# Optimization experiments

Measured on AMD Instinct MI355X. Metric: run time of the kernel, lower is better.

## Reference

```python
import jax, jax.numpy as jnp
import numpy as np

NUM_HEADS = 16
EPS = 1e-12  # matches torch F.normalize eps


def _l2_normalize(x):
    n = jnp.sqrt(jnp.sum(x * x, axis=-1, keepdims=True))
    return x / jnp.maximum(n, EPS)


def setup_inputs() -> dict:
    key = jax.random.key(0)
    ks = jax.random.split(key, 9)
    B, L, S, D = 4, 4096, 4096, 1024
    s = 1.0 / np.sqrt(D)
    return {
        "q": jax.random.normal(ks[0], (B, L, D), jnp.float32),
        "k": jax.random.normal(ks[1], (B, S, D), jnp.float32),
        "v": jax.random.normal(ks[2], (B, S, D), jnp.float32),
        "Wq": jax.random.normal(ks[3], (D, D), jnp.float32) * s,
        "bq": jax.random.normal(ks[4], (D,), jnp.float32) * 0.01,
        "Wk": jax.random.normal(ks[5], (D, D), jnp.float32) * s,
        "bk": jax.random.normal(ks[6], (D,), jnp.float32) * 0.01,
        "Wv": jax.random.normal(ks[7], (D, D), jnp.float32) * s,
        "bv": jax.random.normal(ks[8], (D,), jnp.float32) * 0.01,
    }


def reference(q, k, v, Wq, bq, Wk, bk, Wv, bv):
    B = q.shape[0]
    H = NUM_HEADS
    # Linear projections (torch Linear: x @ W^T + b)
    qp = q @ Wq.T + bq  # [B, L, D]
    kp = k @ Wk.T + bk  # [B, S, D]
    vp = v @ Wv.T + bv  # [B, S, D]
    # Split heads: [B, T, H, i] -> [B, H, T, i]
    def split(x):
        Bx, T, D = x.shape
        return x.reshape(Bx, T, H, D // H).transpose(0, 2, 1, 3)
    qh = split(qp)
    kh = _l2_normalize(split(kp))
    vh = _l2_normalize(split(vp))
    # No softmax -> exact reassociation: (q k^T) v == q (k^T v)
    kv = jnp.einsum('bhsi,bhsj->bhij', kh, vh)  # [B, H, i, i]
    xh = jnp.einsum('bhli,bhij->bhlj', qh, kv)  # [B, H, L, i]
    # Merge heads: [B, H, L, i] -> [B, L, H*i]
    Bx, Hh, L, I = xh.shape
    return xh.transpose(0, 2, 1, 3).reshape(Bx, L, Hh * I)
```

## Files before the change

kernel.cpp:

```cpp
#include <hip/hip_runtime.h>
#include <hip/hip_bf16.h>
#include <stdint.h>

typedef __attribute__((ext_vector_type(8))) short bf16x8;
typedef __attribute__((ext_vector_type(4))) float f32x4;
typedef __attribute__((ext_vector_type(8))) unsigned short ushort8;

__device__ __forceinline__ float bf2f(unsigned short u) {
  union { unsigned int i; float f; } x; x.i = ((unsigned int)u) << 16; return x.f;
}
__device__ __forceinline__ unsigned short f2bf(float f) {
  union { __hip_bfloat16 h; unsigned short u; } x; x.h = __float2bfloat16(f); return x.u;
}

__device__ __forceinline__ void gload_lds16(const void* g, void* l) {
  __builtin_amdgcn_global_load_lds((__attribute__((address_space(1))) const void*)g,
                                   (__attribute__((address_space(3))) void*)l, 16, 0, 0);
}

__global__ __launch_bounds__(256) void cvt3_kernel(const float* __restrict__ a,
                                                   const float* __restrict__ b,
                                                   const float* __restrict__ c,
                                                   unsigned short* __restrict__ oa,
                                                   unsigned short* __restrict__ ob,
                                                   unsigned short* __restrict__ oc,
                                                   int n8) {
  const float* in = blockIdx.y == 0 ? a : blockIdx.y == 1 ? b : c;
  unsigned short* out = blockIdx.y == 0 ? oa : blockIdx.y == 1 ? ob : oc;
  int i = blockIdx.x * 256 + threadIdx.x;
  if (i >= n8) return;
  const float4* p = (const float4*)(in + (size_t)i * 8);
  float4 x = p[0], y = p[1];
  ushort8 o;
  o[0] = f2bf(x.x); o[1] = f2bf(x.y); o[2] = f2bf(x.z); o[3] = f2bf(x.w);
  o[4] = f2bf(y.x); o[5] = f2bf(y.y); o[6] = f2bf(y.z); o[7] = f2bf(y.w);
  *(ushort8*)(out + (size_t)i * 8) = o;
}

__device__ __forceinline__ void gemm256_loop(
    const unsigned short* __restrict__ A,
    const unsigned short* __restrict__ B,
    int bm, int bn,
    unsigned short (*As)[256][32], unsigned short (*Bs)[256][32],
    f32x4 (*acc)[4]) {
  const int tid = threadIdx.x;
  const int widx = tid >> 6, lane = tid & 63;
  const int wr = widx >> 2, wc = widx & 3;
  const int fr = lane & 15, fkg = lane >> 4;
  const int pgo = (fkg ^ ((fr >> 1) & 3)) * 8;
  const int srow = lane >> 2;
  const int sg = ((lane & 3) ^ ((lane >> 3) & 3)) * 8;

  const size_t abase = (size_t)(bm * 256) * 1024;
  const size_t bbase = (size_t)(bn * 256) * 1024;

  bf16x8 aF[8], bF[4];

#define STG_A(bufi, kh, kt)                                                                \
  {                                                                                        \
    gload_lds16(A + abase + (size_t)(widx * 16 + srow) * 1024 + (kt) * 64 + (kh) * 32 + sg,\
                &As[(bufi) * 2 + (kh)][widx * 16][0]);                                     \
    gload_lds16(A + abase + (size_t)(128 + widx * 16 + srow) * 1024 + (kt) * 64 + (kh) * 32 + sg, \
                &As[(bufi) * 2 + (kh)][128 + widx * 16][0]);                               \
  }
#define STG_B(bufi, kh, kt)                                                                \
  {                                                                                        \
    gload_lds16(B + bbase + (size_t)(widx * 16 + srow) * 1024 + (kt) * 64 + (kh) * 32 + sg,\
                &Bs[(bufi) * 2 + (kh)][widx * 16][0]);                                     \
    gload_lds16(B + bbase + (size_t)(128 + widx * 16 + srow) * 1024 + (kt) * 64 + (kh) * 32 + sg, \
                &Bs[(bufi) * 2 + (kh)][128 + widx * 16][0]);                               \
  }
#define LDA(bufi, ks)                                                                      \
  _Pragma("unroll") for (int m = 0; m < 8; ++m)                                            \
      aF[m] = *(const bf16x8*)&As[(bufi) * 2 + (ks)][wr * 128 + m * 16 + fr][pgo];
#define LDBALL(bufi, ks)                                                                   \
  _Pragma("unroll") for (int n = 0; n < 4; ++n)                                            \
      bF[n] = *(const bf16x8*)&Bs[(bufi) * 2 + (ks)][wc * 64 + n * 16 + fr][pgo];
#define MMALL()                                                                            \
  {                                                                                        \
    __builtin_amdgcn_s_setprio(1);                                                         \
    _Pragma("unroll") for (int m = 0; m < 8; ++m)                                          \
        _Pragma("unroll") for (int n = 0; n < 4; ++n)                                      \
            acc[m][n] = __builtin_amdgcn_mfma_f32_16x16x32_bf16(aF[m], bF[n], acc[m][n], 0, 0, 0); \
    __builtin_amdgcn_s_setprio(0);                                                         \
  }
#define BARM() asm volatile("s_barrier" ::: "memory")
#define VMW(N) asm volatile("s_waitcnt vmcnt(" #N ")" ::: "memory")

  STG_A(0, 0, 0); STG_B(0, 0, 0);
  STG_A(0, 1, 0); STG_B(0, 1, 0);
  STG_A(1, 0, 1); STG_B(1, 0, 1);
  VMW(4);
  BARM();

  for (int i = 0; i < 8; ++i) {
    const int t1s = 2 * i + 1, u0 = 2 * i + 2, u1 = 2 * i + 3;
    const bool st = (i < 7);
    LDA(0, 0); LDBALL(0, 0); STG_A(1, 1, t1s); STG_B(1, 1, t1s);
    MMALL(); BARM();
    LDA(0, 1); LDBALL(0, 1); if (st) { STG_A(0, 0, u0); STG_B(0, 0, u0); }
    MMALL();
    if (st) { VMW(4); } else { VMW(0); }
    BARM();
    LDA(1, 0); LDBALL(1, 0); if (st) { STG_A(0, 1, u0); STG_B(0, 1, u0); }
    MMALL(); BARM();
    LDA(1, 1); LDBALL(1, 1); if (st) { STG_A(1, 0, u1); STG_B(1, 0, u1); }
    MMALL();
    if (st) { VMW(4); } else { VMW(0); }
    BARM();
  }
#undef STG_A
#undef STG_B
#undef LDA
#undef LDBALL
#undef MMALL
#undef BARM
#undef VMW
}

__global__ __launch_bounds__(512, 1) void proj_norm_kernel(
    const unsigned short* __restrict__ A0, const unsigned short* __restrict__ A1,
    const unsigned short* __restrict__ B0, const unsigned short* __restrict__ B1,
    const float* __restrict__ bias0, const float* __restrict__ bias1,
    unsigned short* __restrict__ C0, unsigned short* __restrict__ C1) {
  __shared__ unsigned short As[4][256][32];
  __shared__ unsigned short Bs[4][256][32];
  const int flat = (blockIdx.z * 64 + blockIdx.y) * 4 + blockIdx.x;
  const int swz = (flat & 7) * 64 + (flat >> 3);
  const int zz = swz >> 8;
  const int rem = swz & 255;
  const int bm = rem >> 2, bn = rem & 3;
  const unsigned short* A = zz ? A1 : A0;
  const unsigned short* B = zz ? B1 : B0;
  const float* bias = zz ? bias1 : bias0;
  unsigned short* C = zz ? C1 : C0;

  f32x4 acc[8][4];
#pragma unroll
  for (int m = 0; m < 8; ++m)
#pragma unroll
    for (int n = 0; n < 4; ++n) acc[m][n] = (f32x4){0.f, 0.f, 0.f, 0.f};

  gemm256_loop(A, B, bm, bn, As, Bs, acc);

  const int tid = threadIdx.x, widx = tid >> 6, lane = tid & 63;
  const int wr = widx >> 2, wc = widx & 3;
  const int fr = lane & 15, g4 = (lane >> 4) * 4;

  float bsv[4];
#pragma unroll
  for (int n = 0; n < 4; ++n) bsv[n] = bias[bn * 256 + wc * 64 + n * 16 + fr];
#pragma unroll
  for (int m = 0; m < 8; ++m) {
    float val[4][4];
    float inv[4];
#pragma unroll
    for (int j = 0; j < 4; ++j) {
      float s = 0.f;
#pragma unroll
      for (int n = 0; n < 4; ++n) {
        val[n][j] = acc[m][n][j] + bsv[n];
        s += val[n][j] * val[n][j];
      }
      s += __shfl_xor(s, 1); s += __shfl_xor(s, 2);
      s += __shfl_xor(s, 4); s += __shfl_xor(s, 8);
      inv[j] = 1.f / fmaxf(sqrtf(s), 1e-12f);
    }
#pragma unroll
    for (int n = 0; n < 4; ++n) {
      const int col = bn * 256 + wc * 64 + n * 16 + fr;
#pragma unroll
      for (int j = 0; j < 4; ++j) {
        const int row = bm * 256 + wr * 128 + m * 16 + g4 + j;
        C[(size_t)row * 1024 + col] = f2bf(val[n][j] * inv[j]);
      }
    }
  }
}

__global__ __launch_bounds__(512, 1) void final_fold_kernel(
    const unsigned short* __restrict__ A,
    const unsigned short* __restrict__ Wqb,
    const float* __restrict__ bq,
    const unsigned short* __restrict__ kvT,
    float* __restrict__ out) {
  __shared__ __align__(16) unsigned char smem[163840];
  unsigned short (*As)[256][32] = (unsigned short (*)[256][32])smem;
  unsigned short (*Bs)[256][32] = (unsigned short (*)[256][32])(smem + 65536);

  const int flat = blockIdx.y * 4 + blockIdx.x;
  const int swz = (flat & 7) * 32 + (flat >> 3);
  const int bm = swz >> 2, bn = swz & 3;
  const int bB = bm >> 4;

  const int tid = threadIdx.x, widx = tid >> 6, lane = tid & 63;
  const int wr = widx >> 2, wc = widx & 3;
  const int fr = lane & 15, fkg = lane >> 4, g4 = fkg * 4;

#pragma unroll
  for (int t = 0; t < 4; ++t) {
    int unit = t * 512 + tid;
    int h = unit >> 9;
    int jr = (unit >> 3) & 63;
    int g = unit & 7;
    ushort8 vvv = *(const ushort8*)(kvT +
        ((size_t)(bB * 16 + bn * 4 + h) * 4096) + jr * 64 + g * 8);
    *(ushort8*)(smem + 131072 + h * 8192 + jr * 128 + ((g ^ (jr & 7)) * 16)) = vvv;
  }
  __syncthreads();

  f32x4 acc[8][4];
#pragma unroll
  for (int m = 0; m < 8; ++m)
#pragma unroll
    for (int n = 0; n < 4; ++n) acc[m][n] = (f32x4){0.f, 0.f, 0.f, 0.f};

  gemm256_loop(A, Wqb, bm, bn, As, Bs, acc);

  {
    float bsv[4];
#pragma unroll
    for (int n = 0; n < 4; ++n) bsv[n] = bq[bn * 256 + wc * 64 + n * 16 + fr];
#pragma unroll
    for (int m = 0; m < 8; ++m)
#pragma unroll
      for (int n = 0; n < 4; ++n)
#pragma unroll
        for (int j = 0; j < 4; ++j) {
          float v = acc[m][n][j] + bsv[n];
          int r = m * 16 + g4 + j;
          int c = n * 16 + fr;
          *(unsigned short*)(smem + widx * 16384 + r * 128 +
                             (((c >> 3) ^ (r & 7)) * 16) + (c & 7) * 2) = f2bf(v);
        }
  }
  __syncthreads();

  f32x4 acc2[8][4];
#pragma unroll
  for (int m = 0; m < 8; ++m)
#pragma unroll
    for (int n = 0; n < 4; ++n) acc2[m][n] = (f32x4){0.f, 0.f, 0.f, 0.f};

#pragma unroll
  for (int ks = 0; ks < 2; ++ks) {
    bf16x8 a2[8], b2[4];
#pragma unroll
    for (int m = 0; m < 8; ++m)
      a2[m] = *(const bf16x8*)(smem + widx * 16384 + (m * 16 + fr) * 128 +
                               (((ks * 4 + fkg) ^ (fr & 7)) * 16));
#pragma unroll
    for (int n = 0; n < 4; ++n)
      b2[n] = *(const bf16x8*)(smem + 131072 + wc * 8192 + (n * 16 + fr) * 128 +
                               (((ks * 4 + fkg) ^ (fr & 7)) * 16));
#pragma unroll
    for (int m = 0; m < 8; ++m)
#pragma unroll
      for (int n = 0; n < 4; ++n)
        acc2[m][n] = __builtin_amdgcn_mfma_f32_16x16x32_bf16(a2[m], b2[n], acc2[m][n], 0, 0, 0);
  }

#pragma unroll
  for (int n = 0; n < 4; ++n) {
    const int col = bn * 256 + wc * 64 + n * 16 + fr;
#pragma unroll
    for (int m = 0; m < 8; ++m)
#pragma unroll
      for (int j = 0; j < 4; ++j) {
        const int row = bm * 256 + wr * 128 + m * 16 + g4 + j;
        out[(size_t)row * 1024 + col] = acc2[m][n][j];
      }
  }
}

__global__ __launch_bounds__(256) void kv_part_kernel(const unsigned short* __restrict__ kh,
                                                      const unsigned short* __restrict__ vh,
                                                      float* __restrict__ kvp) {
  const int chunk = blockIdx.x, h = blockIdx.y, b = blockIdx.z;
  __shared__ unsigned short khT[64][264];
  __shared__ unsigned short vhT[64][264];
  const int tid = threadIdx.x, wid = tid >> 6, lane = tid & 63;
  const int fr = lane & 15, fk = (lane >> 4) * 8, g4 = (lane >> 4) * 4;

  const int jb = tid & 7, sb = tid >> 3;
  const size_t base = ((size_t)b * 4096 + chunk * 256) * 1024 + h * 64;
  {
    ushort8 rk[8], rv[8];
#pragma unroll
    for (int u = 0; u < 8; ++u) {
      rk[u] = *(const ushort8*)(kh + base + (size_t)(sb * 8 + u) * 1024 + jb * 8);
      rv[u] = *(const ushort8*)(vh + base + (size_t)(sb * 8 + u) * 1024 + jb * 8);
    }
#pragma unroll
    for (int jj = 0; jj < 8; ++jj) {
      ushort8 ck, cv;
#pragma unroll
      for (int u = 0; u < 8; ++u) { ck[u] = rk[u][jj]; cv[u] = rv[u][jj]; }
      *(ushort8*)&khT[jb * 8 + jj][sb * 8] = ck;
      *(ushort8*)&vhT[jb * 8 + jj][sb * 8] = cv;
    }
  }
  __syncthreads();

  f32x4 acc2[4];
#pragma unroll
  for (int n = 0; n < 4; ++n) acc2[n] = (f32x4){0.f, 0.f, 0.f, 0.f};
#pragma unroll
  for (int ks = 0; ks < 8; ++ks) {
    bf16x8 a2 = *(const bf16x8*)&khT[wid * 16 + fr][ks * 32 + fk];
    bf16x8 b2[4];
#pragma unroll
    for (int jt = 0; jt < 4; ++jt) b2[jt] = *(const bf16x8*)&vhT[jt * 16 + fr][ks * 32 + fk];
#pragma unroll
    for (int jt = 0; jt < 4; ++jt)
      acc2[jt] = __builtin_amdgcn_mfma_f32_16x16x32_bf16(a2, b2[jt], acc2[jt], 0, 0, 0);
  }
  float* dst = kvp + ((size_t)chunk * 64 + b * 16 + h) * 4096;
#pragma unroll
  for (int jt = 0; jt < 4; ++jt)
#pragma unroll
    for (int jj = 0; jj < 4; ++jj)
      dst[(wid * 16 + g4 + jj) * 64 + jt * 16 + fr] = acc2[jt][jj];
}

__global__ __launch_bounds__(256) void kvt_reduce_kernel(const float* __restrict__ kvp,
                                                         unsigned short* __restrict__ kvT) {
  const int bh = blockIdx.x;
  for (int e = threadIdx.x; e < 4096; e += 256) {
    float s = 0.f;
#pragma unroll
    for (int c = 0; c < 16; ++c) s += kvp[((size_t)c * 64 + bh) * 4096 + e];
    int i = e >> 6, j = e & 63;
    kvT[(size_t)bh * 4096 + j * 64 + i] = f2bf(s);
  }
}

extern "C" void kernel_launch(void* const* d_in, const int* in_sizes, int n_in,
                              void* d_out, int out_size, void* d_ws, size_t ws_size,
                              hipStream_t stream) {
  const float* q = (const float*)d_in[0];
  const float* k = (const float*)d_in[1];
  const float* v = (const float*)d_in[2];
  const float* Wq = (const float*)d_in[3];
  const float* bq = (const float*)d_in[4];
  const float* Wk = (const float*)d_in[5];
  const float* bk = (const float*)d_in[6];
  const float* Wv = (const float*)d_in[7];
  const float* bv = (const float*)d_in[8];
  float* out = (float*)d_out;

  const size_t NE = (size_t)16384 * 1024;
  const size_t MB = 1048576;

  char* ws = (char*)d_ws;
  unsigned short* kbf = (unsigned short*)(ws + 0 * MB);
  unsigned short* qbf = (unsigned short*)(ws + 32 * MB);
  unsigned short* kh = (unsigned short*)(ws + 64 * MB);
  unsigned short* vh = (unsigned short*)(ws + 96 * MB);
  unsigned short* vbf = (unsigned short*)(ws + 64 * MB);
  unsigned short* Wqb = (unsigned short*)(ws + 128 * MB);
  unsigned short* Wkb = (unsigned short*)(ws + 130 * MB);
  unsigned short* Wvb = (unsigned short*)(ws + 132 * MB);
  unsigned short* kvT = (unsigned short*)(ws + 134 * MB);
  float* kvp = (float*)kbf;

  (void)vbf;

  unsigned short* kbf_ = (unsigned short*)(ws + 0 * MB);
  unsigned short* vbf_ = (unsigned short*)(ws + 32 * MB);
  unsigned short* qbf_ = vbf_;

  cvt3_kernel<<<dim3(8192, 2), 256, 0, stream>>>(k, v, v, kbf_, vbf_, vbf_, (int)(NE / 8));
  cvt3_kernel<<<dim3(512, 3), 256, 0, stream>>>(Wq, Wk, Wv, Wqb, Wkb, Wvb, 131072);

  proj_norm_kernel<<<dim3(4, 64, 2), 512, 0, stream>>>(kbf_, vbf_, Wkb, Wvb, bk, bv, kh, vh);

  cvt3_kernel<<<dim3(8192, 1), 256, 0, stream>>>(q, q, q, qbf_, qbf_, qbf_, (int)(NE / 8));

  kv_part_kernel<<<dim3(16, 16, 4), 256, 0, stream>>>(kh, vh, kvp);

  kvt_reduce_kernel<<<64, 256, 0, stream>>>(kvp, kvT);

  final_fold_kernel<<<dim3(4, 64), 512, 0, stream>>>(qbf_, Wqb, bq, kvT, out);
}
```

Baseline: 212.0 us.

## Rewrite projection+norm GEMM with simple double-buffered LDS loop

Replaces the shared 4-stage hand-scheduled gemm256_loop in proj_norm_kernel with a standalone 2-buffer loop. Each iteration issues the next tile's direct global-to-LDS loads, then does fragment reads and MFMAs under raised priority, with one barrier per k-step. LDS use drops from 4 stages to 2. The new loads also drop the XOR swizzle, so fragment reads may hit LDS bank conflicts. The launch bound asks for 4 blocks per CU, which will not fit given the large accumulator register use. Host code is only tidied, with pointer aliases renamed.

```diff
diff --git a/kernel.cpp b/kernel.cpp
--- a/kernel.cpp
+++ b/kernel.cpp
@@ -37,6 +37,103 @@
   *(ushort8*)(out + (size_t)i * 8) = o;
 }
 
+__global__ __launch_bounds__(512, 4) void proj_norm_kernel(
+    const unsigned short* __restrict__ A0, const unsigned short* __restrict__ A1,
+    const unsigned short* __restrict__ B0, const unsigned short* __restrict__ B1,
+    const float* __restrict__ bias0, const float* __restrict__ bias1,
+    unsigned short* __restrict__ C0, unsigned short* __restrict__ C1) {
+  __shared__ unsigned short As[2][256][32];
+  __shared__ unsigned short Bs[2][256][32];
+
+  const int flat = (blockIdx.z * 64 + blockIdx.y) * 4 + blockIdx.x;
+  const int swz = (flat & 7) * 64 + (flat >> 3);
+  const int zz = swz >> 8;
+  const int rem = swz & 255;
+  const int bm = rem >> 2, bn = rem & 3;
+  const unsigned short* A = zz ? A1 : A0;
+  const unsigned short* B = zz ? B1 : B0;
+  const float* bias = zz ? bias1 : bias0;
+  unsigned short* C = zz ? C1 : C0;
+
+  const int tid = threadIdx.x, widx = tid >> 6, lane = tid & 63;
+  const int wr = widx >> 2, wc = widx & 3;
+  const int fr = lane & 15, fkg = lane >> 4, g4 = fkg * 4;
+  const int srow = lane >> 2;
+  const int sgr = (lane & 3) * 8;
+
+  const size_t abase = (size_t)(bm * 256) * 1024;
+  const size_t bbase = (size_t)(bn * 256) * 1024;
+
+  f32x4 acc[8][4];
+#pragma unroll
+  for (int m = 0; m < 8; ++m)
+#pragma unroll
+    for (int n = 0; n < 4; ++n) acc[m][n] = (f32x4){0.f, 0.f, 0.f, 0.f};
+
+#define STG(buf, kt)                                                                       \
+  _Pragma("unroll") for (int cc = 0; cc < 2; ++cc) {                                       \
+    const int r0 = cc * 128 + widx * 16;                                                   \
+    gload_lds16(A + abase + (size_t)(r0 + srow) * 1024 + (kt) * 32 + sgr,                  \
+                &As[buf][r0][0]);                                                          \
+    gload_lds16(B + bbase + (size_t)(r0 + srow) * 1024 + (kt) * 32 + sgr,                  \
+                &Bs[buf][r0][0]);                                                          \
+  }
+
+  STG(0, 0);
+  __syncthreads();
+
+  for (int t = 0; t < 32; ++t) {
+    const int cur = t & 1;
+    if (t < 31) { STG(cur ^ 1, t + 1); }
+    bf16x8 aF[8], bF[4];
+#pragma unroll
+    for (int m = 0; m < 8; ++m)
+      aF[m] = *(const bf16x8*)&As[cur][wr * 128 + m * 16 + fr][fkg * 8];
+#pragma unroll
+    for (int n = 0; n < 4; ++n)
+      bF[n] = *(const bf16x8*)&Bs[cur][wc * 64 + n * 16 + fr][fkg * 8];
+    __builtin_amdgcn_s_setprio(1);
+#pragma unroll
+    for (int m = 0; m < 8; ++m)
+#pragma unroll
+      for (int n = 0; n < 4; ++n)
+        acc[m][n] = __builtin_amdgcn_mfma_f32_16x16x32_bf16(aF[m], bF[n], acc[m][n], 0, 0, 0);
+    __builtin_amdgcn_s_setprio(0);
+    __syncthreads();
+  }
+#undef STG
+
+  float bsv[4];
+#pragma unroll
+  for (int n = 0; n < 4; ++n) bsv[n] = bias[bn * 256 + wc * 64 + n * 16 + fr];
+#pragma unroll
+  for (int m = 0; m < 8; ++m) {
+    float val[4][4];
+    float inv[4];
+#pragma unroll
+    for (int j = 0; j < 4; ++j) {
+      float s = 0.f;
+#pragma unroll
+      for (int n = 0; n < 4; ++n) {
+        val[n][j] = acc[m][n][j] + bsv[n];
+        s += val[n][j] * val[n][j];
+      }
+      s += __shfl_xor(s, 1); s += __shfl_xor(s, 2);
+      s += __shfl_xor(s, 4); s += __shfl_xor(s, 8);
+      inv[j] = 1.f / fmaxf(sqrtf(s), 1e-12f);
+    }
+#pragma unroll
+    for (int n = 0; n < 4; ++n) {
+      const int col = bn * 256 + wc * 64 + n * 16 + fr;
+#pragma unroll
+      for (int j = 0; j < 4; ++j) {
+        const int row = bm * 256 + wr * 128 + m * 16 + g4 + j;
+        C[(size_t)row * 1024 + col] = f2bf(val[n][j] * inv[j]);
+      }
+    }
+  }
+}
+
 __device__ __forceinline__ void gemm256_loop(
     const unsigned short* __restrict__ A,
     const unsigned short* __restrict__ B,
@@ -118,66 +215,6 @@
 #undef VMW
 }
 
-__global__ __launch_bounds__(512, 1) void proj_norm_kernel(
-    const unsigned short* __restrict__ A0, const unsigned short* __restrict__ A1,
-    const unsigned short* __restrict__ B0, const unsigned short* __restrict__ B1,
-    const float* __restrict__ bias0, const float* __restrict__ bias1,
-    unsigned short* __restrict__ C0, unsigned short* __restrict__ C1) {
-  __shared__ unsigned short As[4][256][32];
-  __shared__ unsigned short Bs[4][256][32];
-  const int flat = (blockIdx.z * 64 + blockIdx.y) * 4 + blockIdx.x;
-  const int swz = (flat & 7) * 64 + (flat >> 3);
-  const int zz = swz >> 8;
-  const int rem = swz & 255;
-  const int bm = rem >> 2, bn = rem & 3;
-  const unsigned short* A = zz ? A1 : A0;
-  const unsigned short* B = zz ? B1 : B0;
-  const float* bias = zz ? bias1 : bias0;
-  unsigned short* C = zz ? C1 : C0;
-
-  f32x4 acc[8][4];
-#pragma unroll
-  for (int m = 0; m < 8; ++m)
-#pragma unroll
-    for (int n = 0; n < 4; ++n) acc[m][n] = (f32x4){0.f, 0.f, 0.f, 0.f};
-
-  gemm256_loop(A, B, bm, bn, As, Bs, acc);
-
-  const int tid = threadIdx.x, widx = tid >> 6, lane = tid & 63;
-  const int wr = widx >> 2, wc = widx & 3;
-  const int fr = lane & 15, g4 = (lane >> 4) * 4;
-
-  float bsv[4];
-#pragma unroll
-  for (int n = 0; n < 4; ++n) bsv[n] = bias[bn * 256 + wc * 64 + n * 16 + fr];
-#pragma unroll
-  for (int m = 0; m < 8; ++m) {
-    float val[4][4];
-    float inv[4];
-#pragma unroll
-    for (int j = 0; j < 4; ++j) {
-      float s = 0.f;
-#pragma unroll
-      for (int n = 0; n < 4; ++n) {
-        val[n][j] = acc[m][n][j] + bsv[n];
-        s += val[n][j] * val[n][j];
-      }
-      s += __shfl_xor(s, 1); s += __shfl_xor(s, 2);
-      s += __shfl_xor(s, 4); s += __shfl_xor(s, 8);
-      inv[j] = 1.f / fmaxf(sqrtf(s), 1e-12f);
-    }
-#pragma unroll
-    for (int n = 0; n < 4; ++n) {
-      const int col = bn * 256 + wc * 64 + n * 16 + fr;
-#pragma unroll
-      for (int j = 0; j < 4; ++j) {
-        const int row = bm * 256 + wr * 128 + m * 16 + g4 + j;
-        C[(size_t)row * 1024 + col] = f2bf(val[n][j] * inv[j]);
-      }
-    }
-  }
-}
-
 __global__ __launch_bounds__(512, 1) void final_fold_kernel(
     const unsigned short* __restrict__ A,
     const unsigned short* __restrict__ Wqb,
@@ -354,32 +391,26 @@
 
   char* ws = (char*)d_ws;
   unsigned short* kbf = (unsigned short*)(ws + 0 * MB);
-  unsigned short* qbf = (unsigned short*)(ws + 32 * MB);
+  unsigned short* vbf = (unsigned short*)(ws + 32 * MB);
   unsigned short* kh = (unsigned short*)(ws + 64 * MB);
   unsigned short* vh = (unsigned short*)(ws + 96 * MB);
-  unsigned short* vbf = (unsigned short*)(ws + 64 * MB);
   unsigned short* Wqb = (unsigned short*)(ws + 128 * MB);
   unsigned short* Wkb = (unsigned short*)(ws + 130 * MB);
   unsigned short* Wvb = (unsigned short*)(ws + 132 * MB);
   unsigned short* kvT = (unsigned short*)(ws + 134 * MB);
   float* kvp = (float*)kbf;
-
-  (void)vbf;
-
-  unsigned short* kbf_ = (unsigned short*)(ws + 0 * MB);
-  unsigned short* vbf_ = (unsigned short*)(ws + 32 * MB);
-  unsigned short* qbf_ = vbf_;
-
-  cvt3_kernel<<<dim3(8192, 2), 256, 0, stream>>>(k, v, v, kbf_, vbf_, vbf_, (int)(NE / 8));
+  unsigned short* qbf = vbf;
+
+  cvt3_kernel<<<dim3(8192, 2), 256, 0, stream>>>(k, v, v, kbf, vbf, vbf, (int)(NE / 8));
   cvt3_kernel<<<dim3(512, 3), 256, 0, stream>>>(Wq, Wk, Wv, Wqb, Wkb, Wvb, 131072);
 
-  proj_norm_kernel<<<dim3(4, 64, 2), 512, 0, stream>>>(kbf_, vbf_, Wkb, Wvb, bk, bv, kh, vh);
-
-  cvt3_kernel<<<dim3(8192, 1), 256, 0, stream>>>(q, q, q, qbf_, qbf_, qbf_, (int)(NE / 8));
+  proj_norm_kernel<<<dim3(4, 64, 2), 512, 0, stream>>>(kbf, vbf, Wkb, Wvb, bk, bv, kh, vh);
+
+  cvt3_kernel<<<dim3(8192, 1), 256, 0, stream>>>(q, q, q, qbf, qbf, qbf, (int)(NE / 8));
 
   kv_part_kernel<<<dim3(16, 16, 4), 256, 0, stream>>>(kh, vh, kvp);
 
   kvt_reduce_kernel<<<64, 256, 0, stream>>>(kvp, kvT);
 
-  final_fold_kernel<<<dim3(4, 64), 512, 0, stream>>>(qbf_, Wqb, bq, kvT, out);
-}
+  final_fold_kernel<<<dim3(4, 64), 512, 0, stream>>>(qbf, Wqb, bq, kvT, out);
+}
```

New measurement: 742.6 us. 3.5x slower.
